# Performance work log

Hardware: AMD Instinct MI355X
Metric: run time of the kernel (lower is better)

Reference implementation:

```python
import jax, jax.numpy as jnp
import numpy as np

B, L, D, H = 48, 512, 192, 6
DK = D // H
HID = 4 * D
EPS = 1e-5
SCALE = 1.0 / np.float32(np.sqrt(DK))


def _ln(x, g, b):
    mu = x.mean(-1, keepdims=True)
    v = ((x - mu) ** 2).mean(-1, keepdims=True)
    return (x - mu) * jax.lax.rsqrt(v + EPS) * g + b


def _mln(x, m, g, b):
    # masked layernorm: valid rows normalized, invalid rows pass through unchanged
    return jnp.where(m[..., None], _ln(x, g, b), x)


def _mha(q, k, v, mask, wq, bq, wk, bk, wv, bv, wo, bo):
    def proj(x, w, bb):
        return (x @ w + bb).reshape(B, L, H, DK).transpose(0, 2, 1, 3)  # [B,H,L,dk]
    Q, K, V = proj(q, wq, bq), proj(k, wk, bk), proj(v, wv, bv)
    s = jnp.einsum('bhqd,bhkd->bhqk', Q, K) * SCALE
    s = jnp.where(mask[:, None], -1e9, s)  # mask True = invalid pair
    p = jax.nn.softmax(s, axis=-1)
    o = jnp.einsum('bhqk,bhkd->bhqd', p, V).transpose(0, 2, 1, 3).reshape(B, L, D)
    return o @ wo + bo


def _forward(x_a, x_b, valid_a, valid_b,
             ln_a_g, ln_a_b, ln_b_g, ln_b_b, ln_oa_g, ln_oa_b, ln_ob_g, ln_ob_b,
             wq, bq, wk, bk, wv, bv, wo, bo,
             fln_g, fln_b, flno_g, flno_b, w1, b1, w2, b2):
    mB2A = ~(valid_a[:, :, None] & valid_b[:, None, :])  # [B,La,Lb]
    mA2B = ~(valid_b[:, :, None] & valid_a[:, None, :])
    a = _mln(x_a, valid_a, ln_a_g, ln_a_b)
    b = _mln(x_b, valid_b, ln_b_g, ln_b_b)
    oa = _mha(a, b, b, mB2A, wq, bq, wk, bk, wv, bv, wo, bo)
    oa = _mln(oa + x_a, valid_a, ln_oa_g, ln_oa_b)
    ob = _mha(b, a, a, mA2B, wq, bq, wk, bk, wv, bv, wo, bo)
    ob = _mln(ob + x_b, valid_b, ln_ob_g, ln_ob_b)

    def ffn(x, m):
        xn = _mln(x, m, fln_g, fln_b)
        y = jax.nn.gelu(xn @ w1 + b1, approximate=False) @ w2 + b2
        return _mln(x + y, m, flno_g, flno_b)

    return ffn(oa, valid_a), ffn(ob, valid_b)


def setup_inputs() -> dict:
    key = jax.random.key(0)
    ks = jax.random.split(key, 12)
    p = lambda k, s: jax.random.normal(k, s, dtype=jnp.float32) * 0.02
    ones = lambda s: jnp.ones(s, dtype=jnp.float32)
    zeros = lambda s: jnp.zeros(s, dtype=jnp.float32)
    return {
        'x_a': jax.random.normal(ks[0], (B, L, D), dtype=jnp.float32),
        'x_b': jax.random.normal(ks[1], (B, L, D), dtype=jnp.float32),
        'valid_a': jax.random.bernoulli(ks[2], 0.9, (B, L)),
        'valid_b': jax.random.bernoulli(ks[3], 0.9, (B, L)),
        'ln_a_g': ones((D,)), 'ln_a_b': zeros((D,)),
        'ln_b_g': ones((D,)), 'ln_b_b': zeros((D,)),
        'ln_oa_g': ones((D,)), 'ln_oa_b': zeros((D,)),
        'ln_ob_g': ones((D,)), 'ln_ob_b': zeros((D,)),
        'wq': p(ks[4], (D, D)), 'bq': zeros((D,)),
        'wk': p(ks[5], (D, D)), 'bk': zeros((D,)),
        'wv': p(ks[6], (D, D)), 'bv': zeros((D,)),
        'wo': p(ks[7], (D, D)), 'bo': zeros((D,)),
        'fln_g': ones((D,)), 'fln_b': zeros((D,)),
        'flno_g': ones((D,)), 'flno_b': zeros((D,)),
        'w1': p(ks[8], (D, HID)), 'b1': zeros((HID,)),
        'w2': p(ks[9], (HID, D)), 'b2': zeros((D,)),
    }


def reference(x_a, x_b, valid_a, valid_b,
              ln_a_g, ln_a_b, ln_b_g, ln_b_b, ln_oa_g, ln_oa_b, ln_ob_g, ln_ob_b,
              wq, bq, wk, bk, wv, bv, wo, bo,
              fln_g, fln_b, flno_g, flno_b, w1, b1, w2, b2):
    return _forward(x_a, x_b, valid_a, valid_b,
                    ln_a_g, ln_a_b, ln_b_g, ln_b_b, ln_oa_g, ln_oa_b, ln_ob_g, ln_ob_b,
                    wq, bq, wk, bk, wv, bv, wo, bo,
                    fln_g, fln_b, flno_g, flno_b, w1, b1, w2, b2)
```

## Files before the change

### kernel.cpp

```cpp
#include <hip/hip_runtime.h>
#include <math.h>

#define BB 48
#define LL 512
#define DD 192
#define HH 6
#define DKK 32
#define HID 768
#define ROWS (BB * LL)
#define BLD ((size_t)ROWS * DD)
#define SCALE_ATT 0.17677669529663687f
#define SB2 0.25503531f
#define MASKED_X (-36.0f)

typedef unsigned short ushort_t;
typedef unsigned int uint_t;
typedef __bf16 bf16x8 __attribute__((ext_vector_type(8)));
typedef float f32x4 __attribute__((ext_vector_type(4)));

union U4BF8 { uint4 u; bf16x8 b; };
union BFU { __bf16 h; ushort_t u; };

__device__ __forceinline__ ushort_t f2bf(float f) {
  union { float f; uint_t u; } v; v.f = f;
  uint_t r = v.u + 0x7fffu + ((v.u >> 16) & 1u);
  return (ushort_t)(r >> 16);
}
__device__ __forceinline__ float bf2f(ushort_t u) {
  union { uint_t u; float f; } v; v.u = ((uint_t)u) << 16; return v.f;
}
__device__ __forceinline__ ushort_t cvt_bf(float f) {
  BFU c; c.h = (__bf16)f; return c.u;
}

__device__ __forceinline__ int swz_w(int n, int k, int N) {
  return ((k >> 5) * (N >> 4) + (n >> 4)) * 512 +
         ((((k & 31) >> 3) << 4) + (n & 15)) * 8 + (k & 7);
}

__global__ __launch_bounds__(256) void pack_kernel(
    const float* __restrict__ wq, const float* __restrict__ wk,
    const float* __restrict__ wv, const float* __restrict__ wo,
    const float* __restrict__ w1, const float* __restrict__ w2,
    const float* __restrict__ bq, const float* __restrict__ bk,
    const float* __restrict__ bv,
    ushort_t* __restrict__ Wqkv, ushort_t* __restrict__ Wo,
    ushort_t* __restrict__ W1, ushort_t* __restrict__ W2,
    float* __restrict__ bqkv) {
  int i = blockIdx.x * 256 + threadIdx.x;
  if (i < 110592) {
    int n2 = i / 192, k = i - n2 * 192;
    int part = n2 / 192, n = n2 - part * 192;
    const float* src = part == 0 ? wq : (part == 1 ? wk : wv);
    Wqkv[swz_w(n2, k, 576)] = f2bf(src[k * 192 + n]);
  } else if (i < 147456) {
    int j = i - 110592;
    int n = j / 192, k = j - n * 192;
    Wo[swz_w(n, k, 192)] = f2bf(wo[k * 192 + n]);
  } else if (i < 294912) {
    int j = i - 147456;
    int n = j / 192, k = j - n * 192;
    W1[j] = f2bf(w1[k * 768 + n]);
  } else if (i < 442368) {
    int j = i - 294912;
    int n = j / 768, k = j - n * 768;
    W2[j] = f2bf(w2[k * 192 + n]);
  } else if (i < 442944) {
    int j = i - 442368;
    bqkv[j] = j < 192 ? bq[j] : (j < 384 ? bk[j - 192] : bv[j - 384]);
  }
}

__global__ __launch_bounds__(64) void mln2_kernel(
    const float* __restrict__ x0, const float* __restrict__ x1,
    const float* __restrict__ res0, const float* __restrict__ res1,
    const int* __restrict__ v0, const int* __restrict__ v1,
    const float* __restrict__ g0, const float* __restrict__ be0,
    const float* __restrict__ g1, const float* __restrict__ be1,
    float* __restrict__ outf, ushort_t* __restrict__ outb) {
  int row = blockIdx.x;
  int side = row >= ROWS;
  int r = side ? row - ROWS : row;
  int lane = threadIdx.x;
  const float* x = (side ? x1 : x0) + (size_t)r * DD;
  const float* rp = side ? res1 : res0;
  const float* g = side ? g1 : g0;
  const float* be = side ? be1 : be0;
  float v0_ = x[lane], v1_ = x[lane + 64], v2_ = x[lane + 128];
  if (rp != nullptr) {
    const float* rr = rp + (size_t)r * DD;
    v0_ += rr[lane]; v1_ += rr[lane + 64]; v2_ += rr[lane + 128];
  }
  float s = v0_ + v1_ + v2_;
#pragma unroll
  for (int off = 32; off; off >>= 1) s += __shfl_xor(s, off);
  float mu = s * (1.0f / 192.0f);
  float d0 = v0_ - mu, d1 = v1_ - mu, d2 = v2_ - mu;
  float ss = d0 * d0 + d1 * d1 + d2 * d2;
#pragma unroll
  for (int off = 32; off; off >>= 1) ss += __shfl_xor(ss, off);
  float inv = rsqrtf(ss * (1.0f / 192.0f) + 1e-5f);
  float r0, r1, r2;
  if ((side ? v1 : v0)[r]) {
    r0 = d0 * inv * g[lane]       + be[lane];
    r1 = d1 * inv * g[lane + 64]  + be[lane + 64];
    r2 = d2 * inv * g[lane + 128] + be[lane + 128];
  } else {
    r0 = v0_; r1 = v1_; r2 = v2_;
  }
  size_t o = (size_t)row * DD;
  if (outf != nullptr) {
    outf[o + lane] = r0; outf[o + lane + 64] = r1; outf[o + lane + 128] = r2;
  }
  if (outb != nullptr) {
    outb[o + lane] = f2bf(r0); outb[o + lane + 64] = f2bf(r1);
    outb[o + lane + 128] = f2bf(r2);
  }
}

__global__ __launch_bounds__(64) void mln_chain_kernel(
    const float* __restrict__ t,
    const float* __restrict__ res0, const float* __restrict__ res1,
    const int* __restrict__ v0, const int* __restrict__ v1,
    const float* __restrict__ g1a, const float* __restrict__ b1a,
    const float* __restrict__ g1b, const float* __restrict__ b1b,
    const float* __restrict__ g2, const float* __restrict__ b2,
    float* __restrict__ outf, ushort_t* __restrict__ outb) {
  int row = blockIdx.x;
  int side = row >= ROWS;
  int r = side ? row - ROWS : row;
  int lane = threadIdx.x;
  const float* tr = t + (size_t)row * DD;
  const float* rr = (side ? res1 : res0) + (size_t)r * DD;
  const float* g1 = side ? g1b : g1a;
  const float* b1 = side ? b1b : b1a;
  int vld = (side ? v1 : v0)[r];
  float v0_ = tr[lane] + rr[lane];
  float v1_ = tr[lane + 64] + rr[lane + 64];
  float v2_ = tr[lane + 128] + rr[lane + 128];
  float s = v0_ + v1_ + v2_;
#pragma unroll
  for (int off = 32; off; off >>= 1) s += __shfl_xor(s, off);
  float mu = s * (1.0f / 192.0f);
  float d0 = v0_ - mu, d1 = v1_ - mu, d2 = v2_ - mu;
  float ss = d0 * d0 + d1 * d1 + d2 * d2;
#pragma unroll
  for (int off = 32; off; off >>= 1) ss += __shfl_xor(ss, off);
  float inv = rsqrtf(ss * (1.0f / 192.0f) + 1e-5f);
  float y0, y1, y2;
  if (vld) {
    y0 = d0 * inv * g1[lane]       + b1[lane];
    y1 = d1 * inv * g1[lane + 64]  + b1[lane + 64];
    y2 = d2 * inv * g1[lane + 128] + b1[lane + 128];
  } else { y0 = v0_; y1 = v1_; y2 = v2_; }
  size_t o = (size_t)row * DD;
  outf[o + lane] = y0; outf[o + lane + 64] = y1; outf[o + lane + 128] = y2;
  float s2 = y0 + y1 + y2;
#pragma unroll
  for (int off = 32; off; off >>= 1) s2 += __shfl_xor(s2, off);
  float mu2 = s2 * (1.0f / 192.0f);
  float e0 = y0 - mu2, e1 = y1 - mu2, e2 = y2 - mu2;
  float ss2 = e0 * e0 + e1 * e1 + e2 * e2;
#pragma unroll
  for (int off = 32; off; off >>= 1) ss2 += __shfl_xor(ss2, off);
  float inv2 = rsqrtf(ss2 * (1.0f / 192.0f) + 1e-5f);
  float z0, z1, z2;
  if (vld) {
    z0 = e0 * inv2 * g2[lane]       + b2[lane];
    z1 = e1 * inv2 * g2[lane + 64]  + b2[lane + 64];
    z2 = e2 * inv2 * g2[lane + 128] + b2[lane + 128];
  } else { z0 = y0; z1 = y1; z2 = y2; }
  outb[o + lane] = f2bf(z0); outb[o + lane + 64] = f2bf(z1);
  outb[o + lane + 128] = f2bf(z2);
}

template <int NT, int F32OUT>
__global__ __launch_bounds__(256) void gemm_rowblk_kernel(
    const ushort_t* __restrict__ A, const ushort_t* __restrict__ Wsw,
    const float* __restrict__ bias, float* __restrict__ Cf,
    ushort_t* __restrict__ Cb) {
  constexpr int N = NT * 64;
  constexpr int CSB = N + 8;
  constexpr int CSF = N + 4;
  constexpr int AS_SH = 32 * 200;
  constexpr int CS_SH = F32OUT ? 32 * CSF * 2 : 32 * CSB;
  constexpr int SMEM_SH = AS_SH > CS_SH ? AS_SH : CS_SH;
  __shared__ ushort_t smem[SMEM_SH];
  ushort_t* As = smem;

  int tid = threadIdx.x;
  int w = tid >> 6, lane = tid & 63, l15 = lane & 15, kq = lane >> 4;
  int row0 = blockIdx.x * 32;

  {
    const ushort_t* ap = A + (size_t)row0 * 192;
#pragma unroll
    for (int i = 0; i < 3; ++i) {
      int idx = tid + i * 256;
      int r = idx / 24, c = (idx - r * 24) * 8;
      *(uint4*)(&As[r * 200 + c]) = *(const uint4*)(ap + idx * 8);
    }
  }
  __syncthreads();

  f32x4 acc[2][NT];
#pragma unroll
  for (int qs = 0; qs < 2; ++qs)
#pragma unroll
    for (int nt = 0; nt < NT; ++nt) acc[qs][nt] = (f32x4){0.f, 0.f, 0.f, 0.f};

#pragma unroll 1
  for (int kk = 0; kk < 6; ++kk) {
    bf16x8 af[2];
#pragma unroll
    for (int qs = 0; qs < 2; ++qs)
      af[qs] = *(const bf16x8*)(&As[(qs * 16 + l15) * 200 + kk * 32 + kq * 8]);
    const ushort_t* wp =
        Wsw + ((size_t)(kk * (N >> 4) + w * NT) << 9) + lane * 8;
#pragma unroll
    for (int nt = 0; nt < NT; ++nt) {
      U4BF8 wf;
      wf.u = *(const uint4*)(wp + (nt << 9));
#pragma unroll
      for (int qs = 0; qs < 2; ++qs)
        acc[qs][nt] = __builtin_amdgcn_mfma_f32_16x16x32_bf16(
            af[qs], wf.b, acc[qs][nt], 0, 0, 0);
    }
  }
  __syncthreads();

  if (!F32OUT) {
    ushort_t* Cs = smem;
#pragma unroll
    for (int nt = 0; nt < NT; ++nt) {
      int col = (w * NT + nt) * 16 + l15;
      float bb = bias[col];
#pragma unroll
      for (int qs = 0; qs < 2; ++qs)
#pragma unroll
        for (int r = 0; r < 4; ++r)
          Cs[(qs * 16 + kq * 4 + r) * CSB + col] = f2bf(acc[qs][nt][r] + bb);
    }
    __syncthreads();
    constexpr int UPR = (N * 2) / 16;
#pragma unroll
    for (int i = 0; i < (32 * UPR) / 256; ++i) {
      int idx = tid + i * 256;
      int r = idx / UPR, u = idx - r * UPR;
      *(uint4*)(Cb + (size_t)row0 * N + idx * 8) =
          *(const uint4*)(&Cs[r * CSB + u * 8]);
    }
  } else {
    float* Cs = (float*)smem;
#pragma unroll
    for (int nt = 0; nt < NT; ++nt) {
      int col = (w * NT + nt) * 16 + l15;
      float bb = bias[col];
#pragma unroll
      for (int qs = 0; qs < 2; ++qs)
#pragma unroll
        for (int r = 0; r < 4; ++r)
          Cs[(qs * 16 + kq * 4 + r) * CSF + col] = acc[qs][nt][r] + bb;
    }
    __syncthreads();
    constexpr int UPR = (N * 4) / 16;
#pragma unroll
    for (int i = 0; i < (32 * UPR) / 256; ++i) {
      int idx = tid + i * 256;
      int r = idx / UPR, u = idx - r * UPR;
      *(float4*)(Cf + (size_t)row0 * N + idx * 4) =
          *(const float4*)(&Cs[r * CSF + u * 4]);
    }
  }
}

__global__ __launch_bounds__(256, 3) void ffn_fused_kernel(
    const ushort_t* __restrict__ A, const ushort_t* __restrict__ W1t,
    const float* __restrict__ bias1, const ushort_t* __restrict__ W2t,
    const float* __restrict__ bias2, float* __restrict__ C) {
  __shared__ ushort_t As[64 * 200];
  __shared__ ushort_t Hs[2][64 * 72];
  int tid = threadIdx.x;
  int w = tid >> 6;
  int lane = tid & 63;
  int l15 = lane & 15;
  int kq = lane >> 4;
  int row0 = blockIdx.x * 64;

#pragma unroll
  for (int i = 0; i < 6; ++i) {
    int idx = tid + i * 256;
    int r = idx / 24, c = (idx % 24) * 8;
    *(uint4*)(&As[r * 200 + c]) = *(const uint4*)(A + (size_t)(row0 + r) * DD + c);
  }

  const ushort_t* w1p = W1t + (size_t)(w * 16 + l15) * DD + kq * 8;
  const ushort_t* w2p = W2t + (size_t)(w * 48 + l15) * HID + kq * 8;

  U4BF8 w1f[6], w1n[6], w2f[6];
#pragma unroll
  for (int kk = 0; kk < 6; ++kk)
    w1f[kk].u = *(const uint4*)(w1p + kk * 32);

  f32x4 Cacc[4][3];
#pragma unroll
  for (int qs = 0; qs < 4; ++qs)
#pragma unroll
    for (int nt = 0; nt < 3; ++nt) Cacc[qs][nt] = (f32x4){0.f, 0.f, 0.f, 0.f};

  __syncthreads();

  for (int hc = 0; hc < 12; ++hc) {
#pragma unroll
    for (int kk2 = 0; kk2 < 2; ++kk2)
#pragma unroll
      for (int nt = 0; nt < 3; ++nt)
        w2f[kk2 * 3 + nt].u =
            *(const uint4*)(w2p + (size_t)(nt * 16) * HID + hc * 64 + kk2 * 32);

    f32x4 Hacc[4];
#pragma unroll
    for (int qs = 0; qs < 4; ++qs) Hacc[qs] = (f32x4){0.f, 0.f, 0.f, 0.f};
#pragma unroll
    for (int kk = 0; kk < 6; ++kk) {
#pragma unroll
      for (int qs = 0; qs < 4; ++qs) {
        bf16x8 af = *(const bf16x8*)(&As[(qs * 16 + l15) * 200 + kk * 32 + kq * 8]);
        Hacc[qs] = __builtin_amdgcn_mfma_f32_16x16x32_bf16(
            af, w1f[kk].b, Hacc[qs], 0, 0, 0);
      }
    }

    if (hc < 11) {
#pragma unroll
      for (int kk = 0; kk < 6; ++kk)
        w1n[kk].u = *(const uint4*)(w1p + (size_t)(hc + 1) * 64 * DD + kk * 32);
    }

    {
      float bb = bias1[hc * 64 + w * 16 + l15];
      ushort_t* hb = &Hs[hc & 1][0];
#pragma unroll
      for (int qs = 0; qs < 4; ++qs)
#pragma unroll
        for (int r = 0; r < 4; ++r) {
          float x = Hacc[qs][r] + bb;
          x = 0.5f * x * (1.0f + erff(x * 0.70710678118654752f));
          hb[(qs * 16 + kq * 4 + r) * 72 + w * 16 + l15] = f2bf(x);
        }
    }
    __syncthreads();

#pragma unroll
    for (int kk2 = 0; kk2 < 2; ++kk2) {
      bf16x8 hf[4];
#pragma unroll
      for (int qs = 0; qs < 4; ++qs)
        hf[qs] = *(const bf16x8*)(&Hs[hc & 1][(qs * 16 + l15) * 72 + kk2 * 32 + kq * 8]);
#pragma unroll
      for (int nt = 0; nt < 3; ++nt)
#pragma unroll
        for (int qs = 0; qs < 4; ++qs)
          Cacc[qs][nt] = __builtin_amdgcn_mfma_f32_16x16x32_bf16(
              hf[qs], w2f[kk2 * 3 + nt].b, Cacc[qs][nt], 0, 0, 0);
    }

#pragma unroll
    for (int kk = 0; kk < 6; ++kk) w1f[kk] = w1n[kk];
  }

#pragma unroll
  for (int qs = 0; qs < 4; ++qs)
#pragma unroll
    for (int nt = 0; nt < 3; ++nt) {
      int col = w * 48 + nt * 16 + l15;
      float bb = bias2[col];
#pragma unroll
      for (int r = 0; r < 4; ++r) {
        int row = row0 + qs * 16 + kq * 4 + r;
        C[(size_t)row * DD + col] = Cacc[qs][nt][r] + bb;
      }
    }
}

__global__ __launch_bounds__(256) void attn_mfma_kernel(
    const ushort_t* __restrict__ QKV,
    const int* __restrict__ valid_a, const int* __restrict__ valid_b,
    ushort_t* __restrict__ out) {
  int i = blockIdx.x;
  int gid = ((i >> 5) << 3) | (i & 7);
  int qt = (i >> 3) & 3;
  int side = gid >= BB * HH;
  int grem = side ? gid - BB * HH : gid;
  int h = grem % HH;
  int batch = grem / HH;
  int tid = threadIdx.x;
  int w = tid >> 6;
  int lane = tid & 63;
  int l15 = lane & 15;
  int kq = lane >> 4;

  const int* validq = side ? valid_b : valid_a;
  const int* validk = side ? valid_a : valid_b;
  size_t qrow0  = (size_t)side * ROWS + (size_t)batch * LL;
  size_t kvrow0 = (size_t)(1 - side) * ROWS + (size_t)batch * LL;

  __shared__ ushort_t VsT[2][32 * 72];
  __shared__ ushort_t Ps[4][32 * 72];

  int qbase = qt * 128 + w * 32;

  U4BF8 qfrag[2];
#pragma unroll
  for (int qs = 0; qs < 2; ++qs)
    qfrag[qs].u = *(const uint4*)(QKV + (qrow0 + qbase + qs * 16 + l15) * 576 +
                                  h * DKK + kq * 8);

  float sqf[2][4], mq[2][4];
#pragma unroll
  for (int qs = 0; qs < 2; ++qs)
#pragma unroll
    for (int r = 0; r < 4; ++r) {
      int vq = validq[batch * LL + qbase + qs * 16 + kq * 4 + r];
      sqf[qs][r] = vq ? SB2 : 0.0f;
      mq[qs][r]  = vq ? 0.0f : MASKED_X;
    }

  float lsum[2][4];
  f32x4 Oacc[2][2];
#pragma unroll
  for (int qs = 0; qs < 2; ++qs) {
#pragma unroll
    for (int r = 0; r < 4; ++r) lsum[qs][r] = 0.0f;
#pragma unroll
    for (int ds = 0; ds < 2; ++ds) Oacc[qs][ds] = (f32x4){0.f, 0.f, 0.f, 0.f};
  }

  uint4 vv = *(const uint4*)(QKV + (kvrow0 + lane) * 576 + 384 + h * DKK + w * 8);
  U4BF8 kf[4];
  int vki[4];
#pragma unroll
  for (int ks = 0; ks < 4; ++ks) {
    kf[ks].u = *(const uint4*)(QKV + (kvrow0 + ks * 16 + l15) * 576 +
                               192 + h * DKK + kq * 8);
    vki[ks] = validk[batch * LL + ks * 16 + l15];
  }

  for (int c = 0; c < LL; c += 64) {
    int buf = (c >> 6) & 1;
    {
      uint_t uu[4] = {vv.x, vv.y, vv.z, vv.w};
#pragma unroll
      for (int j = 0; j < 4; ++j) {
        VsT[buf][(w * 8 + 2 * j) * 72 + lane]     = (ushort_t)(uu[j] & 0xffffu);
        VsT[buf][(w * 8 + 2 * j + 1) * 72 + lane] = (ushort_t)(uu[j] >> 16);
      }
    }
    uint4 vvn;
    if (c + 64 < LL)
      vvn = *(const uint4*)(QKV + (kvrow0 + c + 64 + lane) * 576 +
                            384 + h * DKK + w * 8);
    __syncthreads();

    f32x4 S[2][4];
#pragma unroll
    for (int ks = 0; ks < 4; ++ks)
#pragma unroll
      for (int qs = 0; qs < 2; ++qs) {
        f32x4 z = (f32x4){0.f, 0.f, 0.f, 0.f};
        S[qs][ks] = __builtin_amdgcn_mfma_f32_16x16x32_bf16(
            qfrag[qs].b, kf[ks].b, z, 0, 0, 0);
      }

    float mkb[4];
#pragma unroll
    for (int ks = 0; ks < 4; ++ks) mkb[ks] = vki[ks] ? 0.0f : MASKED_X;

    U4BF8 kfn[4];
    int vkn[4];
    if (c + 64 < LL) {
#pragma unroll
      for (int ks = 0; ks < 4; ++ks) {
        kfn[ks].u = *(const uint4*)(QKV + (kvrow0 + c + 64 + ks * 16 + l15) * 576 +
                                    192 + h * DKK + kq * 8);
        vkn[ks] = validk[batch * LL + c + 64 + ks * 16 + l15];
      }
    }

#pragma unroll
    for (int qs = 0; qs < 2; ++qs)
#pragma unroll
      for (int ks = 0; ks < 4; ++ks)
#pragma unroll
        for (int r = 0; r < 4; ++r) {
          float xs = fmaf(S[qs][ks][r], sqf[qs][r], fminf(mq[qs][r], mkb[ks]));
          float p = __builtin_amdgcn_exp2f(xs);
          lsum[qs][r] += p;
          Ps[w][(qs * 16 + kq * 4 + r) * 72 + ks * 16 + l15] = cvt_bf(p);
        }

#pragma unroll
    for (int kh = 0; kh < 2; ++kh) {
      bf16x8 pf[2], vf[2];
#pragma unroll
      for (int qs = 0; qs < 2; ++qs)
        pf[qs] = *(const bf16x8*)(&Ps[w][(qs * 16 + l15) * 72 + kh * 32 + kq * 8]);
#pragma unroll
      for (int ds = 0; ds < 2; ++ds)
        vf[ds] = *(const bf16x8*)(&VsT[buf][(ds * 16 + l15) * 72 + kh * 32 + kq * 8]);
#pragma unroll
      for (int qs = 0; qs < 2; ++qs)
#pragma unroll
        for (int ds = 0; ds < 2; ++ds)
          Oacc[qs][ds] = __builtin_amdgcn_mfma_f32_16x16x32_bf16(
              pf[qs], vf[ds], Oacc[qs][ds], 0, 0, 0);
    }

    vv = vvn;
#pragma unroll
    for (int ks = 0; ks < 4; ++ks) { kf[ks] = kfn[ks]; vki[ks] = vkn[ks]; }
  }

#pragma unroll
  for (int qs = 0; qs < 2; ++qs)
#pragma unroll
    for (int r = 0; r < 4; ++r) {
      float sm = lsum[qs][r];
#pragma unroll
      for (int off = 1; off < 16; off <<= 1) sm += __shfl_xor(sm, off);
      lsum[qs][r] = sm;
    }

#pragma unroll
  for (int qs = 0; qs < 2; ++qs)
#pragma unroll
    for (int ds = 0; ds < 2; ++ds)
#pragma unroll
      for (int r = 0; r < 4; ++r) {
        int q = qbase + qs * 16 + kq * 4 + r;
        out[(qrow0 + q) * DD + h * DKK + ds * 16 + l15] =
            f2bf(Oacc[qs][ds][r] / lsum[qs][r]);
      }
}

extern "C" void kernel_launch(void* const* d_in, const int* in_sizes, int n_in,
                              void* d_out, int out_size, void* d_ws, size_t ws_size,
                              hipStream_t stream) {
  const float* x_a = (const float*)d_in[0];
  const float* x_b = (const float*)d_in[1];
  const int* valid_a = (const int*)d_in[2];
  const int* valid_b = (const int*)d_in[3];
  const float* ln_a_g = (const float*)d_in[4];
  const float* ln_a_b = (const float*)d_in[5];
  const float* ln_b_g = (const float*)d_in[6];
  const float* ln_b_b = (const float*)d_in[7];
  const float* ln_oa_g = (const float*)d_in[8];
  const float* ln_oa_b = (const float*)d_in[9];
  const float* ln_ob_g = (const float*)d_in[10];
  const float* ln_ob_b = (const float*)d_in[11];
  const float* wq = (const float*)d_in[12];
  const float* bq = (const float*)d_in[13];
  const float* wk = (const float*)d_in[14];
  const float* bk = (const float*)d_in[15];
  const float* wv = (const float*)d_in[16];
  const float* bv = (const float*)d_in[17];
  const float* wo = (const float*)d_in[18];
  const float* bo = (const float*)d_in[19];
  const float* fln_g = (const float*)d_in[20];
  const float* fln_b = (const float*)d_in[21];
  const float* flno_g = (const float*)d_in[22];
  const float* flno_b = (const float*)d_in[23];
  const float* w1 = (const float*)d_in[24];
  const float* b1 = (const float*)d_in[25];
  const float* w2 = (const float*)d_in[26];
  const float* b2 = (const float*)d_in[27];

  char* wsb = (char*)d_ws;
  ushort_t* Wqkv = (ushort_t*)wsb;
  ushort_t* Wo_t = Wqkv + 110592;
  ushort_t* W1_t = Wo_t + 36864;
  ushort_t* W2_t = W1_t + 147456;
  float*    bqkv = (float*)(W2_t + 147456);
  ushort_t* lnFull = (ushort_t*)(wsb + 887040);
  ushort_t* attO   = lnFull;
  ushort_t* QKV = (ushort_t*)(wsb + 19761408);
  float* tmp = (float*)(wsb + 76384512);

  float* out_a = (float*)d_out;

  dim3 b64(64), b128(128), b256(256);
  dim3 gMln(2 * ROWS);
  dim3 gGemm(2 * ROWS / 32);
  dim3 gAttn(BB * HH * 4 * 2);
  dim3 gFFN(2 * ROWS / 64);

  hipLaunchKernelGGL(pack_kernel, dim3(1731), b256, 0, stream,
                     wq, wk, wv, wo, w1, w2, bq, bk, bv,
                     Wqkv, Wo_t, W1_t, W2_t, bqkv);

  hipLaunchKernelGGL(mln2_kernel, gMln, b64, 0, stream,
                     x_a, x_b, (const float*)nullptr, (const float*)nullptr,
                     valid_a, valid_b, ln_a_g, ln_a_b, ln_b_g, ln_b_b,
                     (float*)nullptr, lnFull);

  hipLaunchKernelGGL((gemm_rowblk_kernel<9, 0>), gGemm, b256, 0, stream,
                     lnFull, Wqkv, bqkv, (float*)nullptr, QKV);

  hipLaunchKernelGGL(attn_mfma_kernel, gAttn, b256, 0, stream,
                     QKV, valid_a, valid_b, attO);

  hipLaunchKernelGGL((gemm_rowblk_kernel<3, 1>), gGemm, b256, 0, stream,
                     attO, Wo_t, bo, tmp, (ushort_t*)nullptr);

  hipLaunchKernelGGL(mln_chain_kernel, gMln, b64, 0, stream,
                     tmp, x_a, x_b, valid_a, valid_b,
                     ln_oa_g, ln_oa_b, ln_ob_g, ln_ob_b, fln_g, fln_b,
                     out_a, lnFull);

  hipLaunchKernelGGL(ffn_fused_kernel, gFFN, b256, 0, stream,
                     lnFull, W1_t, b1, W2_t, b2, tmp);

  hipLaunchKernelGGL(mln2_kernel, gMln, b64, 0, stream,
                     tmp, tmp + BLD, out_a, out_a + BLD,
                     valid_a, valid_b, flno_g, flno_b, flno_g, flno_b,
                     out_a, (ushort_t*)nullptr);
}
```

Baseline: 362.3 us.

## Fuse masked layernorms into QKV, output-projection and FFN GEMM kernels

```diff
diff --git a/kernel.cpp b/kernel.cpp
--- a/kernel.cpp
+++ b/kernel.cpp
@@ -9,7 +9,6 @@
 #define HID 768
 #define ROWS (BB * LL)
 #define BLD ((size_t)ROWS * DD)
-#define SCALE_ATT 0.17677669529663687f
 #define SB2 0.25503531f
 #define MASKED_X (-36.0f)
 
@@ -25,9 +24,6 @@
   union { float f; uint_t u; } v; v.f = f;
   uint_t r = v.u + 0x7fffu + ((v.u >> 16) & 1u);
   return (ushort_t)(r >> 16);
-}
-__device__ __forceinline__ float bf2f(ushort_t u) {
-  union { uint_t u; float f; } v; v.u = ((uint_t)u) << 16; return v.f;
 }
 __device__ __forceinline__ ushort_t cvt_bf(float f) {
   BFU c; c.h = (__bf16)f; return c.u;
@@ -71,129 +67,126 @@
   }
 }
 
-__global__ __launch_bounds__(64) void mln2_kernel(
-    const float* __restrict__ x0, const float* __restrict__ x1,
-    const float* __restrict__ res0, const float* __restrict__ res1,
-    const int* __restrict__ v0, const int* __restrict__ v1,
-    const float* __restrict__ g0, const float* __restrict__ be0,
-    const float* __restrict__ g1, const float* __restrict__ be1,
-    float* __restrict__ outf, ushort_t* __restrict__ outb) {
-  int row = blockIdx.x;
-  int side = row >= ROWS;
-  int r = side ? row - ROWS : row;
-  int lane = threadIdx.x;
-  const float* x = (side ? x1 : x0) + (size_t)r * DD;
-  const float* rp = side ? res1 : res0;
-  const float* g = side ? g1 : g0;
-  const float* be = side ? be1 : be0;
-  float v0_ = x[lane], v1_ = x[lane + 64], v2_ = x[lane + 128];
-  if (rp != nullptr) {
-    const float* rr = rp + (size_t)r * DD;
-    v0_ += rr[lane]; v1_ += rr[lane + 64]; v2_ += rr[lane + 128];
-  }
-  float s = v0_ + v1_ + v2_;
-#pragma unroll
-  for (int off = 32; off; off >>= 1) s += __shfl_xor(s, off);
-  float mu = s * (1.0f / 192.0f);
-  float d0 = v0_ - mu, d1 = v1_ - mu, d2 = v2_ - mu;
-  float ss = d0 * d0 + d1 * d1 + d2 * d2;
-#pragma unroll
-  for (int off = 32; off; off >>= 1) ss += __shfl_xor(ss, off);
-  float inv = rsqrtf(ss * (1.0f / 192.0f) + 1e-5f);
-  float r0, r1, r2;
-  if ((side ? v1 : v0)[r]) {
-    r0 = d0 * inv * g[lane]       + be[lane];
-    r1 = d1 * inv * g[lane + 64]  + be[lane + 64];
-    r2 = d2 * inv * g[lane + 128] + be[lane + 128];
-  } else {
-    r0 = v0_; r1 = v1_; r2 = v2_;
-  }
-  size_t o = (size_t)row * DD;
-  if (outf != nullptr) {
-    outf[o + lane] = r0; outf[o + lane + 64] = r1; outf[o + lane + 128] = r2;
-  }
-  if (outb != nullptr) {
-    outb[o + lane] = f2bf(r0); outb[o + lane + 64] = f2bf(r1);
-    outb[o + lane + 128] = f2bf(r2);
-  }
-}
-
-__global__ __launch_bounds__(64) void mln_chain_kernel(
-    const float* __restrict__ t,
-    const float* __restrict__ res0, const float* __restrict__ res1,
-    const int* __restrict__ v0, const int* __restrict__ v1,
-    const float* __restrict__ g1a, const float* __restrict__ b1a,
-    const float* __restrict__ g1b, const float* __restrict__ b1b,
-    const float* __restrict__ g2, const float* __restrict__ b2,
-    float* __restrict__ outf, ushort_t* __restrict__ outb) {
-  int row = blockIdx.x;
-  int side = row >= ROWS;
-  int r = side ? row - ROWS : row;
-  int lane = threadIdx.x;
-  const float* tr = t + (size_t)row * DD;
-  const float* rr = (side ? res1 : res0) + (size_t)r * DD;
-  const float* g1 = side ? g1b : g1a;
-  const float* b1 = side ? b1b : b1a;
-  int vld = (side ? v1 : v0)[r];
-  float v0_ = tr[lane] + rr[lane];
-  float v1_ = tr[lane + 64] + rr[lane + 64];
-  float v2_ = tr[lane + 128] + rr[lane + 128];
-  float s = v0_ + v1_ + v2_;
-#pragma unroll
-  for (int off = 32; off; off >>= 1) s += __shfl_xor(s, off);
-  float mu = s * (1.0f / 192.0f);
-  float d0 = v0_ - mu, d1 = v1_ - mu, d2 = v2_ - mu;
-  float ss = d0 * d0 + d1 * d1 + d2 * d2;
-#pragma unroll
-  for (int off = 32; off; off >>= 1) ss += __shfl_xor(ss, off);
-  float inv = rsqrtf(ss * (1.0f / 192.0f) + 1e-5f);
-  float y0, y1, y2;
-  if (vld) {
-    y0 = d0 * inv * g1[lane]       + b1[lane];
-    y1 = d1 * inv * g1[lane + 64]  + b1[lane + 64];
-    y2 = d2 * inv * g1[lane + 128] + b1[lane + 128];
-  } else { y0 = v0_; y1 = v1_; y2 = v2_; }
-  size_t o = (size_t)row * DD;
-  outf[o + lane] = y0; outf[o + lane + 64] = y1; outf[o + lane + 128] = y2;
-  float s2 = y0 + y1 + y2;
-#pragma unroll
-  for (int off = 32; off; off >>= 1) s2 += __shfl_xor(s2, off);
-  float mu2 = s2 * (1.0f / 192.0f);
-  float e0 = y0 - mu2, e1 = y1 - mu2, e2 = y2 - mu2;
-  float ss2 = e0 * e0 + e1 * e1 + e2 * e2;
-#pragma unroll
-  for (int off = 32; off; off >>= 1) ss2 += __shfl_xor(ss2, off);
-  float inv2 = rsqrtf(ss2 * (1.0f / 192.0f) + 1e-5f);
-  float z0, z1, z2;
-  if (vld) {
-    z0 = e0 * inv2 * g2[lane]       + b2[lane];
-    z1 = e1 * inv2 * g2[lane + 64]  + b2[lane + 64];
-    z2 = e2 * inv2 * g2[lane + 128] + b2[lane + 128];
-  } else { z0 = y0; z1 = y1; z2 = y2; }
-  outb[o + lane] = f2bf(z0); outb[o + lane + 64] = f2bf(z1);
-  outb[o + lane + 128] = f2bf(z2);
-}
-
-template <int NT, int F32OUT>
-__global__ __launch_bounds__(256) void gemm_rowblk_kernel(
-    const ushort_t* __restrict__ A, const ushort_t* __restrict__ Wsw,
-    const float* __restrict__ bias, float* __restrict__ Cf,
+__global__ __launch_bounds__(256) void qkv_ln_kernel(
+    const float* __restrict__ xa, const float* __restrict__ xb,
+    const int* __restrict__ va, const int* __restrict__ vb,
+    const float* __restrict__ g_a, const float* __restrict__ b_a,
+    const float* __restrict__ g_b, const float* __restrict__ b_b,
+    const ushort_t* __restrict__ Wsw, const float* __restrict__ bias,
     ushort_t* __restrict__ Cb) {
-  constexpr int N = NT * 64;
+  constexpr int N = 576;
   constexpr int CSB = N + 8;
-  constexpr int CSF = N + 4;
-  constexpr int AS_SH = 32 * 200;
-  constexpr int CS_SH = F32OUT ? 32 * CSF * 2 : 32 * CSB;
-  constexpr int SMEM_SH = AS_SH > CS_SH ? AS_SH : CS_SH;
-  __shared__ ushort_t smem[SMEM_SH];
+  __shared__ ushort_t smem[32 * CSB];
   ushort_t* As = smem;
 
   int tid = threadIdx.x;
   int w = tid >> 6, lane = tid & 63, l15 = lane & 15, kq = lane >> 4;
   int row0 = blockIdx.x * 32;
+  int side = row0 >= ROWS;
+  int rb = row0 - side * ROWS;
 
   {
-    const ushort_t* ap = A + (size_t)row0 * 192;
+    int row = tid >> 3, l8 = tid & 7;
+    const float* xr = (side ? xb : xa) + (size_t)(rb + row) * DD + l8 * 24;
+    float v[24];
+    float s = 0.f;
+#pragma unroll
+    for (int j = 0; j < 6; ++j) {
+      float4 q = *(const float4*)(xr + j * 4);
+      v[j*4+0] = q.x; v[j*4+1] = q.y; v[j*4+2] = q.z; v[j*4+3] = q.w;
+      s += q.x + q.y + q.z + q.w;
+    }
+    s += __shfl_xor(s, 1); s += __shfl_xor(s, 2); s += __shfl_xor(s, 4);
+    float mu = s * (1.0f / 192.0f);
+    float ss = 0.f;
+#pragma unroll
+    for (int j = 0; j < 24; ++j) { float d = v[j] - mu; ss += d * d; }
+    ss += __shfl_xor(ss, 1); ss += __shfl_xor(ss, 2); ss += __shfl_xor(ss, 4);
+    float inv = rsqrtf(ss * (1.0f / 192.0f) + 1e-5f);
+    int vld = (side ? vb : va)[rb + row];
+    const float* g = side ? g_b : g_a;
+    const float* be = side ? b_b : b_a;
+    ushort_t ob[24];
+#pragma unroll
+    for (int j = 0; j < 24; ++j) {
+      int col = l8 * 24 + j;
+      float r = vld ? (v[j] - mu) * inv * g[col] + be[col] : v[j];
+      ob[j] = f2bf(r);
+    }
+#pragma unroll
+    for (int j = 0; j < 3; ++j)
+      *(uint4*)(&As[row * 200 + l8 * 24 + j * 8]) = *(const uint4*)(&ob[j * 8]);
+  }
+  __syncthreads();
+
+  f32x4 acc[2][9];
+#pragma unroll
+  for (int qs = 0; qs < 2; ++qs)
+#pragma unroll
+    for (int nt = 0; nt < 9; ++nt) acc[qs][nt] = (f32x4){0.f, 0.f, 0.f, 0.f};
+
+#pragma unroll 1
+  for (int kk = 0; kk < 6; ++kk) {
+    bf16x8 af[2];
+#pragma unroll
+    for (int qs = 0; qs < 2; ++qs)
+      af[qs] = *(const bf16x8*)(&As[(qs * 16 + l15) * 200 + kk * 32 + kq * 8]);
+    const ushort_t* wp =
+        Wsw + ((size_t)(kk * (N >> 4) + w * 9) << 9) + lane * 8;
+#pragma unroll
+    for (int nt = 0; nt < 9; ++nt) {
+      U4BF8 wf;
+      wf.u = *(const uint4*)(wp + (nt << 9));
+#pragma unroll
+      for (int qs = 0; qs < 2; ++qs)
+        acc[qs][nt] = __builtin_amdgcn_mfma_f32_16x16x32_bf16(
+            af[qs], wf.b, acc[qs][nt], 0, 0, 0);
+    }
+  }
+  __syncthreads();
+
+  ushort_t* Cs = smem;
+#pragma unroll
+  for (int nt = 0; nt < 9; ++nt) {
+    int col = (w * 9 + nt) * 16 + l15;
+    float bb = bias[col];
+#pragma unroll
+    for (int qs = 0; qs < 2; ++qs)
+#pragma unroll
+      for (int r = 0; r < 4; ++r)
+        Cs[(qs * 16 + kq * 4 + r) * CSB + col] = f2bf(acc[qs][nt][r] + bb);
+  }
+  __syncthreads();
+  constexpr int UPR = (N * 2) / 16;
+#pragma unroll
+  for (int i = 0; i < (32 * UPR) / 256; ++i) {
+    int idx = tid + i * 256;
+    int r = idx / UPR, u = idx - r * UPR;
+    *(uint4*)(Cb + (size_t)row0 * N + idx * 8) =
+        *(const uint4*)(&Cs[r * CSB + u * 8]);
+  }
+}
+
+__global__ __launch_bounds__(256) void oproj_ln_kernel(
+    const ushort_t* __restrict__ A, const ushort_t* __restrict__ Wsw,
+    const float* __restrict__ bias,
+    const float* __restrict__ xa, const float* __restrict__ xb,
+    const int* __restrict__ va, const int* __restrict__ vb,
+    const float* __restrict__ g_oa, const float* __restrict__ b_oa,
+    const float* __restrict__ g_ob, const float* __restrict__ b_ob,
+    const float* __restrict__ g_f, const float* __restrict__ b_f,
+    float* __restrict__ outf, ushort_t* __restrict__ outb) {
+  __shared__ float smemf[32 * 196];
+  ushort_t* As = (ushort_t*)smemf;
+
+  int tid = threadIdx.x;
+  int w = tid >> 6, lane = tid & 63, l15 = lane & 15, kq = lane >> 4;
+  int row0 = blockIdx.x * 32;
+  int side = row0 >= ROWS;
+  int rb = row0 - side * ROWS;
+
+  {
+    const ushort_t* ap = A + (size_t)row0 * DD;
 #pragma unroll
     for (int i = 0; i < 3; ++i) {
       int idx = tid + i * 256;
@@ -203,11 +196,11 @@
   }
   __syncthreads();
 
-  f32x4 acc[2][NT];
+  f32x4 acc[2][3];
 #pragma unroll
   for (int qs = 0; qs < 2; ++qs)
 #pragma unroll
-    for (int nt = 0; nt < NT; ++nt) acc[qs][nt] = (f32x4){0.f, 0.f, 0.f, 0.f};
+    for (int nt = 0; nt < 3; ++nt) acc[qs][nt] = (f32x4){0.f, 0.f, 0.f, 0.f};
 
 #pragma unroll 1
   for (int kk = 0; kk < 6; ++kk) {
@@ -216,9 +209,9 @@
     for (int qs = 0; qs < 2; ++qs)
       af[qs] = *(const bf16x8*)(&As[(qs * 16 + l15) * 200 + kk * 32 + kq * 8]);
     const ushort_t* wp =
-        Wsw + ((size_t)(kk * (N >> 4) + w * NT) << 9) + lane * 8;
-#pragma unroll
-    for (int nt = 0; nt < NT; ++nt) {
+        Wsw + ((size_t)(kk * (192 >> 4) + w * 3) << 9) + lane * 8;
+#pragma unroll
+    for (int nt = 0; nt < 3; ++nt) {
       U4BF8 wf;
       wf.u = *(const uint4*)(wp + (nt << 9));
 #pragma unroll
@@ -229,63 +222,96 @@
   }
   __syncthreads();
 
-  if (!F32OUT) {
-    ushort_t* Cs = smem;
-#pragma unroll
-    for (int nt = 0; nt < NT; ++nt) {
-      int col = (w * NT + nt) * 16 + l15;
-      float bb = bias[col];
-#pragma unroll
-      for (int qs = 0; qs < 2; ++qs)
-#pragma unroll
-        for (int r = 0; r < 4; ++r)
-          Cs[(qs * 16 + kq * 4 + r) * CSB + col] = f2bf(acc[qs][nt][r] + bb);
-    }
-    __syncthreads();
-    constexpr int UPR = (N * 2) / 16;
-#pragma unroll
-    for (int i = 0; i < (32 * UPR) / 256; ++i) {
-      int idx = tid + i * 256;
-      int r = idx / UPR, u = idx - r * UPR;
-      *(uint4*)(Cb + (size_t)row0 * N + idx * 8) =
-          *(const uint4*)(&Cs[r * CSB + u * 8]);
-    }
-  } else {
-    float* Cs = (float*)smem;
-#pragma unroll
-    for (int nt = 0; nt < NT; ++nt) {
-      int col = (w * NT + nt) * 16 + l15;
-      float bb = bias[col];
-#pragma unroll
-      for (int qs = 0; qs < 2; ++qs)
-#pragma unroll
-        for (int r = 0; r < 4; ++r)
-          Cs[(qs * 16 + kq * 4 + r) * CSF + col] = acc[qs][nt][r] + bb;
-    }
-    __syncthreads();
-    constexpr int UPR = (N * 4) / 16;
-#pragma unroll
-    for (int i = 0; i < (32 * UPR) / 256; ++i) {
-      int idx = tid + i * 256;
-      int r = idx / UPR, u = idx - r * UPR;
-      *(float4*)(Cf + (size_t)row0 * N + idx * 4) =
-          *(const float4*)(&Cs[r * CSF + u * 4]);
-    }
-  }
+  float* Cs = smemf;
+#pragma unroll
+  for (int nt = 0; nt < 3; ++nt) {
+    int col = (w * 3 + nt) * 16 + l15;
+    float bb = bias[col];
+#pragma unroll
+    for (int qs = 0; qs < 2; ++qs)
+#pragma unroll
+      for (int r = 0; r < 4; ++r)
+        Cs[(qs * 16 + kq * 4 + r) * 196 + col] = acc[qs][nt][r] + bb;
+  }
+  __syncthreads();
+
+  int row = tid >> 3, l8 = tid & 7;
+  int grow = row0 + row;
+  const float* resr = (side ? xb : xa) + (size_t)(rb + row) * DD + l8 * 24;
+  const float* cr = &Cs[row * 196 + l8 * 24];
+  float v[24];
+  float s = 0.f;
+#pragma unroll
+  for (int j = 0; j < 6; ++j) {
+    float4 q = *(const float4*)(resr + j * 4);
+    v[j*4+0] = cr[j*4+0] + q.x; v[j*4+1] = cr[j*4+1] + q.y;
+    v[j*4+2] = cr[j*4+2] + q.z; v[j*4+3] = cr[j*4+3] + q.w;
+    s += v[j*4+0] + v[j*4+1] + v[j*4+2] + v[j*4+3];
+  }
+  s += __shfl_xor(s, 1); s += __shfl_xor(s, 2); s += __shfl_xor(s, 4);
+  float mu = s * (1.0f / 192.0f);
+  float ss = 0.f;
+#pragma unroll
+  for (int j = 0; j < 24; ++j) { float d = v[j] - mu; ss += d * d; }
+  ss += __shfl_xor(ss, 1); ss += __shfl_xor(ss, 2); ss += __shfl_xor(ss, 4);
+  float inv = rsqrtf(ss * (1.0f / 192.0f) + 1e-5f);
+  int vld = (side ? vb : va)[rb + row];
+  const float* g1 = side ? g_ob : g_oa;
+  const float* b1 = side ? b_ob : b_oa;
+  float y[24];
+#pragma unroll
+  for (int j = 0; j < 24; ++j) {
+    int col = l8 * 24 + j;
+    y[j] = vld ? (v[j] - mu) * inv * g1[col] + b1[col] : v[j];
+  }
+  float* op = outf + (size_t)grow * DD + l8 * 24;
+#pragma unroll
+  for (int j = 0; j < 6; ++j) {
+    float4 q = {y[j*4+0], y[j*4+1], y[j*4+2], y[j*4+3]};
+    *(float4*)(op + j * 4) = q;
+  }
+  float s2 = 0.f;
+#pragma unroll
+  for (int j = 0; j < 24; ++j) s2 += y[j];
+  s2 += __shfl_xor(s2, 1); s2 += __shfl_xor(s2, 2); s2 += __shfl_xor(s2, 4);
+  float mu2 = s2 * (1.0f / 192.0f);
+  float ss2 = 0.f;
+#pragma unroll
+  for (int j = 0; j < 24; ++j) { float e = y[j] - mu2; ss2 += e * e; }
+  ss2 += __shfl_xor(ss2, 1); ss2 += __shfl_xor(ss2, 2); ss2 += __shfl_xor(ss2, 4);
+  float inv2 = rsqrtf(ss2 * (1.0f / 192.0f) + 1e-5f);
+  ushort_t zb[24];
+#pragma unroll
+  for (int j = 0; j < 24; ++j) {
+    int col = l8 * 24 + j;
+    float z = vld ? (y[j] - mu2) * inv2 * g_f[col] + b_f[col] : y[j];
+    zb[j] = f2bf(z);
+  }
+  ushort_t* ob = outb + (size_t)grow * DD + l8 * 24;
+#pragma unroll
+  for (int j = 0; j < 3; ++j)
+    *(uint4*)(ob + j * 8) = *(const uint4*)(&zb[j * 8]);
 }
 
 __global__ __launch_bounds__(256, 3) void ffn_fused_kernel(
     const ushort_t* __restrict__ A, const ushort_t* __restrict__ W1t,
     const float* __restrict__ bias1, const ushort_t* __restrict__ W2t,
-    const float* __restrict__ bias2, float* __restrict__ C) {
-  __shared__ ushort_t As[64 * 200];
-  __shared__ ushort_t Hs[2][64 * 72];
+    const float* __restrict__ bias2,
+    const int* __restrict__ va, const int* __restrict__ vb,
+    const float* __restrict__ g_f, const float* __restrict__ b_f,
+    float* __restrict__ outf) {
+  __shared__ float smemf[64 * 196];
+  ushort_t* As = (ushort_t*)smemf;
+  ushort_t* Hs = As + 64 * 200;
+
   int tid = threadIdx.x;
   int w = tid >> 6;
   int lane = tid & 63;
   int l15 = lane & 15;
   int kq = lane >> 4;
   int row0 = blockIdx.x * 64;
+  int side = row0 >= ROWS;
+  int rb0 = row0 - side * ROWS;
 
 #pragma unroll
   for (int i = 0; i < 6; ++i) {
@@ -339,7 +365,7 @@
 
     {
       float bb = bias1[hc * 64 + w * 16 + l15];
-      ushort_t* hb = &Hs[hc & 1][0];
+      ushort_t* hb = &Hs[(hc & 1) * 4608];
 #pragma unroll
       for (int qs = 0; qs < 4; ++qs)
 #pragma unroll
@@ -356,7 +382,8 @@
       bf16x8 hf[4];
 #pragma unroll
       for (int qs = 0; qs < 4; ++qs)
-        hf[qs] = *(const bf16x8*)(&Hs[hc & 1][(qs * 16 + l15) * 72 + kk2 * 32 + kq * 8]);
+        hf[qs] = *(const bf16x8*)(&Hs[(hc & 1) * 4608 +
+                                      (qs * 16 + l15) * 72 + kk2 * 32 + kq * 8]);
 #pragma unroll
       for (int nt = 0; nt < 3; ++nt)
 #pragma unroll
@@ -368,7 +395,9 @@
 #pragma unroll
     for (int kk = 0; kk < 6; ++kk) w1f[kk] = w1n[kk];
   }
-
+  __syncthreads();
+
+  float* Cs = smemf;
 #pragma unroll
   for (int qs = 0; qs < 4; ++qs)
 #pragma unroll
@@ -376,11 +405,43 @@
       int col = w * 48 + nt * 16 + l15;
       float bb = bias2[col];
 #pragma unroll
-      for (int r = 0; r < 4; ++r) {
-        int row = row0 + qs * 16 + kq * 4 + r;
-        C[(size_t)row * DD + col] = Cacc[qs][nt][r] + bb;
-      }
-    }
+      for (int r = 0; r < 4; ++r)
+        Cs[(qs * 16 + kq * 4 + r) * 196 + col] = Cacc[qs][nt][r] + bb;
+    }
+  __syncthreads();
+
+  int row = tid >> 2, l4 = tid & 3;
+  int grow = row0 + row;
+  float* op = outf + (size_t)grow * DD + l4 * 48;
+  const float* cr = &Cs[row * 196 + l4 * 48];
+  float v[48];
+  float s = 0.f;
+#pragma unroll
+  for (int j = 0; j < 12; ++j) {
+    float4 q = *(const float4*)(op + j * 4);
+    v[j*4+0] = cr[j*4+0] + q.x; v[j*4+1] = cr[j*4+1] + q.y;
+    v[j*4+2] = cr[j*4+2] + q.z; v[j*4+3] = cr[j*4+3] + q.w;
+    s += v[j*4+0] + v[j*4+1] + v[j*4+2] + v[j*4+3];
+  }
+  s += __shfl_xor(s, 1); s += __shfl_xor(s, 2);
+  float mu = s * (1.0f / 192.0f);
+  float ss = 0.f;
+#pragma unroll
+  for (int j = 0; j < 48; ++j) { float d = v[j] - mu; ss += d * d; }
+  ss += __shfl_xor(ss, 1); ss += __shfl_xor(ss, 2);
+  float inv = rsqrtf(ss * (1.0f / 192.0f) + 1e-5f);
+  int vld = (side ? vb : va)[rb0 + row];
+#pragma unroll
+  for (int j = 0; j < 12; ++j) {
+    float4 q;
+    float* vv = &v[j * 4];
+#pragma unroll
+    for (int e = 0; e < 4; ++e) {
+      int col = l4 * 48 + j * 4 + e;
+      ((float*)&q)[e] = vld ? (vv[e] - mu) * inv * g_f[col] + b_f[col] : vv[e];
+    }
+    *(float4*)(op + j * 4) = q;
+  }
 }
 
 __global__ __launch_bounds__(256) void attn_mfma_kernel(
@@ -584,12 +645,10 @@
   ushort_t* lnFull = (ushort_t*)(wsb + 887040);
   ushort_t* attO   = lnFull;
   ushort_t* QKV = (ushort_t*)(wsb + 19761408);
-  float* tmp = (float*)(wsb + 76384512);
 
   float* out_a = (float*)d_out;
 
-  dim3 b64(64), b128(128), b256(256);
-  dim3 gMln(2 * ROWS);
+  dim3 b256(256);
   dim3 gGemm(2 * ROWS / 32);
   dim3 gAttn(BB * HH * 4 * 2);
   dim3 gFFN(2 * ROWS / 64);
@@ -598,30 +657,20 @@
                      wq, wk, wv, wo, w1, w2, bq, bk, bv,
                      Wqkv, Wo_t, W1_t, W2_t, bqkv);
 
-  hipLaunchKernelGGL(mln2_kernel, gMln, b64, 0, stream,
-                     x_a, x_b, (const float*)nullptr, (const float*)nullptr,
-                     valid_a, valid_b, ln_a_g, ln_a_b, ln_b_g, ln_b_b,
-                     (float*)nullptr, lnFull);
-
-  hipLaunchKernelGGL((gemm_rowblk_kernel<9, 0>), gGemm, b256, 0, stream,
-                     lnFull, Wqkv, bqkv, (float*)nullptr, QKV);
+  hipLaunchKernelGGL(qkv_ln_kernel, gGemm, b256, 0, stream,
+                     x_a, x_b, valid_a, valid_b,
+                     ln_a_g, ln_a_b, ln_b_g, ln_b_b,
+                     Wqkv, bqkv, QKV);
 
   hipLaunchKernelGGL(attn_mfma_kernel, gAttn, b256, 0, stream,
                      QKV, valid_a, valid_b, attO);
 
-  hipLaunchKernelGGL((gemm_rowblk_kernel<3, 1>), gGemm, b256, 0, stream,
-                     attO, Wo_t, bo, tmp, (ushort_t*)nullptr);
-
-  hipLaunchKernelGGL(mln_chain_kernel, gMln, b64, 0, stream,
-                     tmp, x_a, x_b, valid_a, valid_b,
+  hipLaunchKernelGGL(oproj_ln_kernel, gGemm, b256, 0, stream,
+                     attO, Wo_t, bo, x_a, x_b, valid_a, valid_b,
                      ln_oa_g, ln_oa_b, ln_ob_g, ln_ob_b, fln_g, fln_b,
                      out_a, lnFull);
 
   hipLaunchKernelGGL(ffn_fused_kernel, gFFN, b256, 0, stream,
-                     lnFull, W1_t, b1, W2_t, b2, tmp);
-
-  hipLaunchKernelGGL(mln2_kernel, gMln, b64, 0, stream,
-                     tmp, tmp + BLD, out_a, out_a + BLD,
-                     valid_a, valid_b, flno_g, flno_b, flno_g, flno_b,
-                     out_a, (ushort_t*)nullptr);
-}
+                     lnFull, W1_t, b1, W2_t, b2, valid_a, valid_b,
+                     flno_g, flno_b, out_a);
+}
```

After: 396.0 us. +9.3%, slower.
